# Optimization experiments

Hardware: AMD Instinct MI355X
Metric: run time of the kernel (lower is better)

The kernel has to match this reference:

```python
import jax, jax.numpy as jnp
import numpy as np

N = 100000   # nodes
E = 3200000  # edges (avg degree 32)
G = 512      # graphs in batch
F_IN = 10
H = 30


def setup_inputs() -> dict:
    key = jax.random.key(0)
    ks = jax.random.split(key, 14)
    x = jax.random.normal(ks[0], (N, F_IN), dtype=jnp.float32)
    edge_index = jax.random.randint(ks[1], (2, E), 0, N, dtype=jnp.int64)
    batch = jnp.sort(jax.random.randint(ks[2], (N,), 0, G, dtype=jnp.int64))
    edge_weights = jnp.ones((E,), dtype=jnp.float32)
    s = 0.1
    W1 = jax.random.normal(ks[3], (F_IN, H), jnp.float32) * s
    b1 = jnp.zeros((H,), jnp.float32)
    W2 = jax.random.normal(ks[4], (H, H), jnp.float32) * s
    b2 = jnp.zeros((H,), jnp.float32)
    W3 = jax.random.normal(ks[5], (H, H), jnp.float32) * s
    b3 = jnp.zeros((H,), jnp.float32)
    LW1 = jax.random.normal(ks[6], (H, 10), jnp.float32) * s
    Lb1 = jnp.zeros((10,), jnp.float32)
    LW2 = jax.random.normal(ks[7], (10, 2), jnp.float32) * s
    Lb2 = jnp.zeros((2,), jnp.float32)
    return dict(x=x, edge_index=edge_index, batch=batch, edge_weights=edge_weights,
                W1=W1, b1=b1, W2=W2, b2=b2, W3=W3, b3=b3,
                LW1=LW1, Lb1=Lb1, LW2=LW2, Lb2=Lb2)


def reference(x, edge_index, batch, edge_weights, W1, b1, W2, b2, W3, b3, LW1, Lb1, LW2, Lb2):
    n = x.shape[0]
    row, col = edge_index[0], edge_index[1]
    # PyG gcn_norm: add self-loops with weight 1, symmetric normalization
    loop = jnp.arange(n)
    row_f = jnp.concatenate([row, loop])
    col_f = jnp.concatenate([col, loop])
    w_f = jnp.concatenate([edge_weights, jnp.ones((n,), edge_weights.dtype)])
    deg = jax.ops.segment_sum(w_f, col_f, num_segments=n)
    dis = jnp.where(deg > 0, jax.lax.rsqrt(jnp.where(deg > 0, deg, 1.0)), 0.0)
    norm = dis[row_f] * w_f * dis[col_f]  # [E+N]

    def gcn(h, W, b):
        h = h @ W  # [N, out]
        agg = jax.ops.segment_sum(norm[:, None] * h[row_f], col_f, num_segments=n)
        return agg + b

    h = jax.nn.relu(gcn(x, W1, b1))
    h = jax.nn.relu(gcn(h, W2, b2))
    h = jax.nn.relu(gcn(h, W3, b3))  # embedding [N, 30]
    pooled = jax.ops.segment_max(h, batch, num_segments=G)  # [G, 30]
    out = jax.nn.relu(pooled @ LW1 + Lb1) @ LW2 + Lb2  # [G, 2]
    return out
```

## Files before the change

kernel.cpp:

```cpp
#include <hip/hip_runtime.h>
#include <hip/hip_bf16.h>


#define WG 256
#define CAP 9216
#define T_EDGES 16384

__global__ void k_init(int* bcur, float* pooled, int nb16, int pooledN) {
    int i = blockIdx.x * blockDim.x + threadIdx.x;
    if (i < nb16) bcur[i] = 0;
    if (i < pooledN) pooled[i] = 0.0f;
}

__global__ __launch_bounds__(1024)
void k_bucket(const int* __restrict__ row, const int* __restrict__ col,
              const float* __restrict__ w,
              int* bcur, int2* __restrict__ buck, int E, int NB) {
    __shared__ int hist[512];
    __shared__ int base[512];
    int tid = threadIdx.x;
    for (int i = tid; i < NB; i += 1024) hist[i] = 0;
    __syncthreads();
    int start = blockIdx.x * T_EDGES;
    int end = min(start + T_EDGES, E);
    for (int i = start + tid; i < end; i += 1024)
        atomicAdd(&hist[col[i] >> 8], 1);
    __syncthreads();
    for (int i = tid; i < NB; i += 1024) {
        int h = hist[i];
        base[i] = (h > 0) ? atomicAdd(&bcur[i * 16], h) : 0;
        hist[i] = 0;
    }
    __syncthreads();
    for (int i = start + tid; i < end; i += 1024) {
        int c = col[i];
        int b = c >> 8;
        int off = atomicAdd(&hist[b], 1);
        int pos = base[b] + off;
        if (pos < CAP) {
            int2 pk;
            pk.x = (c & 255) | (row[i] << 8);
            pk.y = __float_as_int(w[i]);
            buck[(size_t)b * CAP + pos] = pk;
        }
    }
}

__global__ __launch_bounds__(1024)
void k_fuse(const int* __restrict__ bcur, const int2* __restrict__ buck,
            float* __restrict__ dis, int* __restrict__ ptr,
            int2* __restrict__ csr, int N, int NB) {
    __shared__ int lc[256];
    __shared__ float lw[256];
    __shared__ int sh[256];
    __shared__ int cur[256];
    __shared__ int sb[512];
    int b = blockIdx.x;
    int tid = threadIdx.x;
    if (tid < 512) sb[tid] = (tid < NB) ? min(bcur[tid * 16], CAP) : 0;
    if (tid < 256) { lc[tid] = 0; lw[tid] = 0.0f; }
    __syncthreads();
    for (int off = 1; off < 512; off <<= 1) {
        int v = (tid < 512 && tid >= off) ? sb[tid - off] : 0;
        __syncthreads();
        if (tid < 512) sb[tid] += v;
        __syncthreads();
    }
    int m = min(bcur[b * 16], CAP);
    int bbase = sb[b] - m;
    if (b == 0 && tid == 0) ptr[N] = sb[511];
    const int2* bp = buck + (size_t)b * CAP;
    for (int i = tid; i < m; i += 1024) {
        int2 pk = bp[i];
        int lcol = pk.x & 255;
        atomicAdd(&lc[lcol], 1);
        atomicAdd(&lw[lcol], __int_as_float(pk.y));
    }
    __syncthreads();
    int lcnt = 0;
    if (tid < 256) { lcnt = lc[tid]; sh[tid] = lcnt; }
    __syncthreads();
    for (int off = 1; off < 256; off <<= 1) {
        int t = (tid >= off && tid < 256) ? sh[tid - off] : 0;
        __syncthreads();
        if (tid < 256) sh[tid] += t;
        __syncthreads();
    }
    int node = (b << 8) + tid;
    if (tid < 256) {
        int base = bbase + sh[tid] - lcnt;
        cur[tid] = base;
        if (node < N) {
            ptr[node] = base;
            float d = 1.0f + lw[tid];
            dis[node] = (d > 0.0f) ? (1.0f / sqrtf(d)) : 0.0f;
        }
    }
    __syncthreads();
    for (int i = tid; i < m; i += 1024) {
        int2 pk = bp[i];
        int lcol = pk.x & 255;
        int pos = atomicAdd(&cur[lcol], 1);
        int2 rec;
        rec.x = (int)(((unsigned)pk.x) >> 8);
        rec.y = pk.y;
        csr[pos] = rec;
    }
}

template <int K>
__global__ void k_matmul(const float* __restrict__ in, int in_stride,
                         const float* __restrict__ W, const float* __restrict__ dis,
                         float* __restrict__ out, int n) {
    __shared__ float Ws[K * 30];
    for (int idx = threadIdx.x; idx < K * 30; idx += blockDim.x) Ws[idx] = W[idx];
    __syncthreads();
    int gid = blockIdx.x * blockDim.x + threadIdx.x;
    int node = gid >> 5;
    int f = gid & 31;
    if (node < n) {
        float acc = 0.0f;
        if (f < 30) {
            const float* ip = in + (size_t)node * in_stride;
#pragma unroll
            for (int k = 0; k < K; k++) acc += ip[k] * Ws[k * 30 + f];
            acc *= dis[node];
        }
        out[(size_t)node * 32 + f] = acc;
    }
}

__global__ void k_agg_fused(const float* __restrict__ hw, const float* __restrict__ dis,
                            const int* __restrict__ ptr, const int2* __restrict__ csr,
                            const float* __restrict__ bias, const float* __restrict__ Wn,
                            float* __restrict__ outw, int n) {
    __shared__ float Ws[30 * 32];
    for (int idx = threadIdx.x; idx < 30 * 32; idx += blockDim.x) {
        int rr = idx >> 5, cc = idx & 31;
        Ws[idx] = (cc < 30) ? Wn[rr * 30 + cc] : 0.0f;
    }
    __syncthreads();
    int wid = (blockIdx.x * blockDim.x + threadIdx.x) >> 6;
    int lane = threadIdx.x & 63;
    if (wid >= n) return;
    int f = lane & 31;
    int half = lane >> 5;
    int s = ptr[wid];
    int e = ptr[wid + 1];
    float acc = 0.0f;
    for (int base = s; base < e; base += 32) {
        int idxv = 0; float nrmv = 0.0f;
        int src = base + lane;
        if (lane < 32 && src < e) {
            int2 v = csr[src];
            idxv = v.x;
            nrmv = __int_as_float(v.y);
        }
#pragma unroll
        for (int j = 0; j < 16; j++) {
            int sl = 2 * j + half;
            int r = __shfl(idxv, sl, 64);
            float w = __shfl(nrmv, sl, 64);
            acc += w * hw[(size_t)r * 32 + f];
        }
    }
    acc += __shfl_xor(acc, 32, 64);
    float dc = dis[wid];
    float r = dc * (acc + hw[(size_t)wid * 32 + f]);
    float bf = (f < 30) ? bias[f] : 0.0f;
    float h = fmaxf(r + bf, 0.0f);
    if (f >= 30) h = 0.0f;
    float o = 0.0f;
#pragma unroll
    for (int k = 0; k < 15; k++) {
        int kk = half * 15 + k;
        float rk = __shfl(h, kk, 64);
        o += rk * Ws[kk * 32 + f];
    }
    o += __shfl_xor(o, 32, 64);
    o *= dc;
    if (half == 0) outw[(size_t)wid * 32 + f] = o;
}

__global__ void k_agg(const float* __restrict__ hw, const float* __restrict__ dis,
                      const int* __restrict__ ptr, const int2* __restrict__ csr,
                      const float* __restrict__ bias,
                      float* __restrict__ out, int n) {
    int wid = (blockIdx.x * blockDim.x + threadIdx.x) >> 6;
    int lane = threadIdx.x & 63;
    if (wid >= n) return;
    int f = lane & 31;
    int half = lane >> 5;
    int s = ptr[wid];
    int e = ptr[wid + 1];
    float acc = 0.0f;
    for (int base = s; base < e; base += 32) {
        int idxv = 0; float nrmv = 0.0f;
        int src = base + lane;
        if (lane < 32 && src < e) {
            int2 v = csr[src];
            idxv = v.x;
            nrmv = __int_as_float(v.y);
        }
#pragma unroll
        for (int j = 0; j < 16; j++) {
            int sl = 2 * j + half;
            int r = __shfl(idxv, sl, 64);
            float w = __shfl(nrmv, sl, 64);
            acc += w * hw[(size_t)r * 32 + f];
        }
    }
    acc += __shfl_xor(acc, 32, 64);
    float dc = dis[wid];
    float r = dc * (acc + hw[(size_t)wid * 32 + f]);
    if (half == 0 && f < 30) {
        r += bias[f];
        out[(size_t)wid * 32 + f] = fmaxf(r, 0.0f);
    }
}

__global__ void k_pool(const float* __restrict__ h, const int* __restrict__ batch,
                       float* pooled, int n) {
    int gid = blockIdx.x * blockDim.x + threadIdx.x;
    int chunk = gid >> 5;
    int f = gid & 31;
    int n0 = chunk * 64;
    if (n0 >= n || f >= 30) return;
    int end = min(n0 + 64, n);
    int curg = batch[n0];
    float m = 0.0f;
    for (int i = n0; i < end; i++) {
        int g = batch[i];
        if (g != curg) {
            atomicMax((int*)&pooled[curg * 32 + f], __float_as_int(m));
            m = 0.0f;
            curg = g;
        }
        m = fmaxf(m, h[(size_t)i * 32 + f]);
    }
    atomicMax((int*)&pooled[curg * 32 + f], __float_as_int(m));
}

__global__ void k_mlp(const float* __restrict__ pooled,
                      const float* __restrict__ LW1, const float* __restrict__ Lb1,
                      const float* __restrict__ LW2, const float* __restrict__ Lb2,
                      float* __restrict__ out, int G) {
    int g = blockIdx.x * blockDim.x + threadIdx.x;
    if (g >= G) return;
    float p[30];
#pragma unroll
    for (int k = 0; k < 30; k++) p[k] = pooled[g * 32 + k];
    float o0 = Lb2[0], o1 = Lb2[1];
#pragma unroll
    for (int j = 0; j < 10; j++) {
        float hj = Lb1[j];
#pragma unroll
        for (int k = 0; k < 30; k++) hj += p[k] * LW1[k * 10 + j];
        hj = fmaxf(hj, 0.0f);
        o0 += hj * LW2[j * 2 + 0];
        o1 += hj * LW2[j * 2 + 1];
    }
    out[g * 2 + 0] = o0;
    out[g * 2 + 1] = o1;
}

extern "C" void kernel_launch(void* const* d_in, const int* in_sizes, int n_in,
                              void* d_out, int out_size, void* d_ws, size_t ws_size,
                              hipStream_t stream) {
    const float* x     = (const float*)d_in[0];
    const int*   ei    = (const int*)d_in[1];
    const int*   batch = (const int*)d_in[2];
    const float* ew    = (const float*)d_in[3];
    const float* W1 = (const float*)d_in[4];  const float* b1  = (const float*)d_in[5];
    const float* W2 = (const float*)d_in[6];  const float* b2  = (const float*)d_in[7];
    const float* W3 = (const float*)d_in[8];  const float* b3  = (const float*)d_in[9];
    const float* LW1 = (const float*)d_in[10]; const float* Lb1 = (const float*)d_in[11];
    const float* LW2 = (const float*)d_in[12]; const float* Lb2 = (const float*)d_in[13];
    float* out = (float*)d_out;

    const int N = in_sizes[2];
    const int E = in_sizes[3];
    const int G = out_size / 2;
    const int* row = ei;
    const int* col = ei + E;

    const int NB = (N + 255) >> 8;

    char* p = (char*)d_ws;
    auto carve = [&](size_t bytes) -> void* {
        void* r = (void*)p;
        p += (bytes + 255) & ~(size_t)255;
        return r;
    };
    int*   ptr       = (int*)carve((size_t)(N + 1) * 4);
    float* dis       = (float*)carve((size_t)N * 4);
    int*   bcur      = (int*)carve((size_t)NB * 16 * 4);
    int2*  csr       = (int2*)carve((size_t)E * 8);
    size_t buckBytes = (size_t)NB * CAP * 8;
    size_t featBytes = (size_t)N * 32 * 4 * 2;
    char*  regionA   = (char*)carve(buckBytes > featBytes ? buckBytes : featBytes);
    int2*  buck      = (int2*)regionA;
    float* bufW      = (float*)regionA;
    float* bufH      = (float*)(regionA + (size_t)N * 32 * 4);
    float* pooled    = (float*)carve((size_t)G * 32 * 4);

    int initN = (NB * 16 > G * 32) ? NB * 16 : G * 32;

    k_init<<<(initN + WG - 1) / WG, WG, 0, stream>>>(bcur, pooled, NB * 16, G * 32);
    k_bucket<<<(E + T_EDGES - 1) / T_EDGES, 1024, 0, stream>>>(row, col, ew, bcur, buck, E, NB);
    k_fuse<<<NB, 1024, 0, stream>>>(bcur, buck, dis, ptr, csr, N, NB);

    int mm_grid  = (int)(((size_t)N * 32 + WG - 1) / WG);
    int agg_grid = (int)(((size_t)N * 64 + WG - 1) / WG);

    k_matmul<10><<<mm_grid, WG, 0, stream>>>(x, 10, W1, dis, bufW, N);
    k_agg_fused<<<agg_grid, WG, 0, stream>>>(bufW, dis, ptr, csr, b1, W2, bufH, N);
    k_agg_fused<<<agg_grid, WG, 0, stream>>>(bufH, dis, ptr, csr, b2, W3, bufW, N);
    k_agg<<<agg_grid, WG, 0, stream>>>(bufW, dis, ptr, csr, b3, bufH, N);

    int pool_grid = (int)((((size_t)(N + 63) / 64) * 32 + WG - 1) / WG);
    k_pool<<<pool_grid, WG, 0, stream>>>(bufH, batch, pooled, N);
    k_mlp<<<(G + WG - 1) / WG, WG, 0, stream>>>(pooled, LW1, Lb1, LW2, Lb2, out, G);
}
```

Baseline: 440.8 us.

## Aggregate raw 10-dim features before first linear layer, reorder layer-2 matmul

```diff
diff --git a/kernel.cpp b/kernel.cpp
--- a/kernel.cpp
+++ b/kernel.cpp
@@ -108,43 +108,22 @@
     }
 }
 
-template <int K>
-__global__ void k_matmul(const float* __restrict__ in, int in_stride,
-                         const float* __restrict__ W, const float* __restrict__ dis,
-                         float* __restrict__ out, int n) {
-    __shared__ float Ws[K * 30];
-    for (int idx = threadIdx.x; idx < K * 30; idx += blockDim.x) Ws[idx] = W[idx];
-    __syncthreads();
+__global__ void k_stage(const float* __restrict__ x, const float* __restrict__ dis,
+                        float* __restrict__ xp, int n) {
     int gid = blockIdx.x * blockDim.x + threadIdx.x;
-    int node = gid >> 5;
-    int f = gid & 31;
-    if (node < n) {
-        float acc = 0.0f;
-        if (f < 30) {
-            const float* ip = in + (size_t)node * in_stride;
-#pragma unroll
-            for (int k = 0; k < K; k++) acc += ip[k] * Ws[k * 30 + f];
-            acc *= dis[node];
-        }
-        out[(size_t)node * 32 + f] = acc;
-    }
-}
-
-__global__ void k_agg_fused(const float* __restrict__ hw, const float* __restrict__ dis,
-                            const int* __restrict__ ptr, const int2* __restrict__ csr,
-                            const float* __restrict__ bias, const float* __restrict__ Wn,
-                            float* __restrict__ outw, int n) {
-    __shared__ float Ws[30 * 32];
-    for (int idx = threadIdx.x; idx < 30 * 32; idx += blockDim.x) {
-        int rr = idx >> 5, cc = idx & 31;
-        Ws[idx] = (cc < 30) ? Wn[rr * 30 + cc] : 0.0f;
-    }
-    __syncthreads();
+    int node = gid >> 4, f = gid & 15;
+    if (node < n)
+        xp[(size_t)node * 16 + f] = (f < 10) ? dis[node] * x[(size_t)node * 10 + f] : 0.0f;
+}
+
+__global__ void k_agg16(const float* __restrict__ xp, const float* __restrict__ dis,
+                        const int* __restrict__ ptr, const int2* __restrict__ csr,
+                        float* __restrict__ y, int n) {
     int wid = (blockIdx.x * blockDim.x + threadIdx.x) >> 6;
     int lane = threadIdx.x & 63;
     if (wid >= n) return;
-    int f = lane & 31;
-    int half = lane >> 5;
+    int f = lane & 15;
+    int q = lane >> 4;
     int s = ptr[wid];
     int e = ptr[wid + 1];
     float acc = 0.0f;
@@ -157,29 +136,74 @@
             nrmv = __int_as_float(v.y);
         }
 #pragma unroll
-        for (int j = 0; j < 16; j++) {
-            int sl = 2 * j + half;
+        for (int j = 0; j < 8; j++) {
+            int sl = 4 * j + q;
             int r = __shfl(idxv, sl, 64);
             float w = __shfl(nrmv, sl, 64);
-            acc += w * hw[(size_t)r * 32 + f];
-        }
-    }
+            acc += w * xp[(size_t)r * 16 + f];
+        }
+    }
+    acc += __shfl_xor(acc, 16, 64);
     acc += __shfl_xor(acc, 32, 64);
     float dc = dis[wid];
-    float r = dc * (acc + hw[(size_t)wid * 32 + f]);
-    float bf = (f < 30) ? bias[f] : 0.0f;
-    float h = fmaxf(r + bf, 0.0f);
-    if (f >= 30) h = 0.0f;
-    float o = 0.0f;
-#pragma unroll
-    for (int k = 0; k < 15; k++) {
-        int kk = half * 15 + k;
-        float rk = __shfl(h, kk, 64);
-        o += rk * Ws[kk * 32 + f];
-    }
-    o += __shfl_xor(o, 32, 64);
-    o *= dc;
-    if (half == 0) outw[(size_t)wid * 32 + f] = o;
+    float r = dc * (acc + xp[(size_t)wid * 16 + f]);
+    if (lane < 16) y[(size_t)wid * 16 + f] = r;
+}
+
+__global__ __launch_bounds__(256)
+void k_lin1(const float* __restrict__ y, const float* __restrict__ W1,
+            const float* __restrict__ b1, const float* __restrict__ W2,
+            const float* __restrict__ dis, float* __restrict__ out, int n) {
+    __shared__ float W1s[10 * 32];
+    __shared__ float W2s[30 * 32];
+    __shared__ float b1s[32];
+    __shared__ float ys[8][16];
+    __shared__ float hs[8][32];
+    int tid = threadIdx.x;
+    for (int i = tid; i < 10 * 32; i += 256) { int k = i >> 5, f = i & 31; W1s[i] = (f < 30) ? W1[k * 30 + f] : 0.0f; }
+    for (int i = tid; i < 30 * 32; i += 256) { int k = i >> 5, f = i & 31; W2s[i] = (f < 30) ? W2[k * 30 + f] : 0.0f; }
+    if (tid < 32) b1s[tid] = (tid < 30) ? b1[tid] : 0.0f;
+    int n8 = tid >> 5, f = tid & 31;
+    int node = blockIdx.x * 8 + n8;
+    __syncthreads();
+    if (node < n && f < 16) ys[n8][f] = y[(size_t)node * 16 + f];
+    __syncthreads();
+    if (node < n) {
+        float h = b1s[f];
+#pragma unroll
+        for (int k = 0; k < 10; k++) h += ys[n8][k] * W1s[k * 32 + f];
+        h = fmaxf(h, 0.0f);
+        if (f >= 30) h = 0.0f;
+        hs[n8][f] = h;
+    }
+    __syncthreads();
+    if (node < n) {
+        float o = 0.0f;
+#pragma unroll
+        for (int k = 0; k < 30; k++) o += hs[n8][k] * W2s[k * 32 + f];
+        out[(size_t)node * 32 + f] = o * dis[node];
+    }
+}
+
+__global__ void k_matmul30(const float* __restrict__ in,
+                           const float* __restrict__ W, const float* __restrict__ dis,
+                           float* __restrict__ out, int n) {
+    __shared__ float Ws[30 * 30];
+    for (int idx = threadIdx.x; idx < 30 * 30; idx += blockDim.x) Ws[idx] = W[idx];
+    __syncthreads();
+    int gid = blockIdx.x * blockDim.x + threadIdx.x;
+    int node = gid >> 5;
+    int f = gid & 31;
+    if (node < n) {
+        float acc = 0.0f;
+        if (f < 30) {
+            const float* ip = in + (size_t)node * 32;
+#pragma unroll
+            for (int k = 0; k < 30; k++) acc += ip[k] * Ws[k * 30 + f];
+            acc *= dis[node];
+        }
+        out[(size_t)node * 32 + f] = acc;
+    }
 }
 
 __global__ void k_agg(const float* __restrict__ hw, const float* __restrict__ dis,
@@ -300,8 +324,10 @@
     size_t featBytes = (size_t)N * 32 * 4 * 2;
     char*  regionA   = (char*)carve(buckBytes > featBytes ? buckBytes : featBytes);
     int2*  buck      = (int2*)regionA;
-    float* bufW      = (float*)regionA;
-    float* bufH      = (float*)(regionA + (size_t)N * 32 * 4);
+    float* bufA      = (float*)regionA;
+    float* xp        = (float*)regionA;
+    float* y16       = (float*)(regionA + (size_t)N * 16 * 4);
+    float* bufB      = (float*)(regionA + (size_t)N * 32 * 4);
     float* pooled    = (float*)carve((size_t)G * 32 * 4);
 
     int initN = (NB * 16 > G * 32) ? NB * 16 : G * 32;
@@ -310,15 +336,17 @@
     k_bucket<<<(E + T_EDGES - 1) / T_EDGES, 1024, 0, stream>>>(row, col, ew, bcur, buck, E, NB);
     k_fuse<<<NB, 1024, 0, stream>>>(bcur, buck, dis, ptr, csr, N, NB);
 
+    int agg_grid = (int)(((size_t)N * 64 + WG - 1) / WG);
     int mm_grid  = (int)(((size_t)N * 32 + WG - 1) / WG);
-    int agg_grid = (int)(((size_t)N * 64 + WG - 1) / WG);
-
-    k_matmul<10><<<mm_grid, WG, 0, stream>>>(x, 10, W1, dis, bufW, N);
-    k_agg_fused<<<agg_grid, WG, 0, stream>>>(bufW, dis, ptr, csr, b1, W2, bufH, N);
-    k_agg_fused<<<agg_grid, WG, 0, stream>>>(bufH, dis, ptr, csr, b2, W3, bufW, N);
-    k_agg<<<agg_grid, WG, 0, stream>>>(bufW, dis, ptr, csr, b3, bufH, N);
+
+    k_stage<<<(int)(((size_t)N * 16 + WG - 1) / WG), WG, 0, stream>>>(x, dis, xp, N);
+    k_agg16<<<agg_grid, WG, 0, stream>>>(xp, dis, ptr, csr, y16, N);
+    k_lin1<<<(N + 7) / 8, 256, 0, stream>>>(y16, W1, b1, W2, dis, bufB, N);
+    k_agg<<<agg_grid, WG, 0, stream>>>(bufB, dis, ptr, csr, b2, bufA, N);
+    k_matmul30<<<mm_grid, WG, 0, stream>>>(bufA, W3, dis, bufB, N);
+    k_agg<<<agg_grid, WG, 0, stream>>>(bufB, dis, ptr, csr, b3, bufA, N);
 
     int pool_grid = (int)((((size_t)(N + 63) / 64) * 32 + WG - 1) / WG);
-    k_pool<<<pool_grid, WG, 0, stream>>>(bufH, batch, pooled, N);
+    k_pool<<<pool_grid, WG, 0, stream>>>(bufA, batch, pooled, N);
     k_mlp<<<(G + WG - 1) / WG, WG, 0, stream>>>(pooled, LW1, Lb1, LW2, Lb2, out, G);
 }
```

After: 416.1 us. -5.6%, faster.
